# Kernel tuning notes

Hardware: AMD Instinct MI355X
Metric: run time of the kernel (lower is better)

The kernel has to match this reference:

```python
import jax, jax.numpy as jnp
import numpy as np

B, T, D = 4, 2048, 1024
H = 16
HD = D // H  # 64

def setup_inputs() -> dict:
    key = jax.random.key(0)
    ks = jax.random.split(key, 5)
    x = jax.random.normal(ks[0], (B, T, D), dtype=jnp.float32)
    # Linear params, torch default init scale ~ U(-1/sqrt(fan_in), 1/sqrt(fan_in))
    s = 1.0 / np.sqrt(D)
    W_qkv = jax.random.uniform(ks[1], (D, 3 * D), jnp.float32, -s, s)
    b_qkv = jax.random.uniform(ks[2], (3 * D,), jnp.float32, -s, s)
    W_proj = jax.random.uniform(ks[3], (D, D), jnp.float32, -s, s)
    b_proj = jax.random.uniform(ks[4], (D,), jnp.float32, -s, s)
    return {"x": x, "W_qkv": W_qkv, "b_qkv": b_qkv, "W_proj": W_proj, "b_proj": b_proj}

def reference(x, W_qkv, b_qkv, W_proj, b_proj):
    b, t, c = x.shape
    qkv = x @ W_qkv + b_qkv                       # [B,T,3D]
    q, k, v = jnp.split(qkv, 3, axis=-1)
    # [B,T,D] -> [B,H,T,HD]
    def heads(a):
        return a.reshape(b, t, H, HD).transpose(0, 2, 1, 3)
    q, k, v = heads(q), heads(k), heads(v)
    scale = 1.0 / jnp.sqrt(jnp.float32(HD))
    att = jnp.einsum('bhqd,bhkd->bhqk', q, k) * scale   # [B,H,T,T]
    causal = jnp.tril(jnp.ones((t, t), dtype=bool))
    att = jnp.where(causal, att, -jnp.inf)
    att = jax.nn.softmax(att, axis=-1)
    out = jnp.einsum('bhqk,bhkd->bhqd', att, v)          # [B,H,T,HD]
    out = out.transpose(0, 2, 1, 3).reshape(b, t, c)
    return out @ W_proj + b_proj
```

## Files before the change

kernel.cpp:

```cpp
#include <hip/hip_runtime.h>
#include <hip/hip_bf16.h>
#include <stdint.h>

using u16 = unsigned short;
using u32t = unsigned int;
typedef __bf16 bf16x8 __attribute__((ext_vector_type(8)));
typedef float f32x4 __attribute__((ext_vector_type(4)));
typedef float f32x16 __attribute__((ext_vector_type(16)));

#define SEQ_T 2048
#define DM 1024
#define NH 16
#define HD 64
#define NB 4

__device__ inline u16 f2bfu(float f) {
    __hip_bfloat16 h = __float2bfloat16(f);
    return __builtin_bit_cast(u16, h);
}

__device__ inline bf16x8 ld_frag(const u16* p) {
    return __builtin_bit_cast(bf16x8, *reinterpret_cast<const uint4*>(p));
}

__device__ inline void gload_lds16(const u16* g, u16* l) {
    __builtin_amdgcn_global_load_lds(
        (const __attribute__((address_space(1))) void*)g,
        (__attribute__((address_space(3))) void*)l, 16, 0, 0);
}

__device__ inline float fexp2(float x) { return __builtin_amdgcn_exp2f(x); }

__global__ __launch_bounds__(256) void prep_kernel(const float* __restrict__ x,
                                                   u16* __restrict__ xb,
                                                   const float* __restrict__ Wqkv,
                                                   u16* __restrict__ wtq,
                                                   const float* __restrict__ Wproj,
                                                   u16* __restrict__ wtp) {
    __shared__ __align__(16) float tile[64][72];
    const int bid = blockIdx.x;
    const int tid = threadIdx.x;
    if (bid < 4096) {
        size_t i = (size_t)bid * 256 + tid;
        const float4* xv = reinterpret_cast<const float4*>(x);
        float4 a = xv[2 * i];
        float4 b = xv[2 * i + 1];
        u16 r[8] = {f2bfu(a.x), f2bfu(a.y), f2bfu(a.z), f2bfu(a.w),
                    f2bfu(b.x), f2bfu(b.y), f2bfu(b.z), f2bfu(b.w)};
        *reinterpret_cast<uint4*>(xb + i * 8) = *reinterpret_cast<const uint4*>(r);
        return;
    }
    const float* W;
    u16* Wt;
    int N, t;
    if (bid < 4864) {
        W = Wqkv; Wt = wtq; N = 3072; t = bid - 4096;
    } else {
        W = Wproj; Wt = wtp; N = 1024; t = bid - 4864;
    }
    const int nbx = N >> 6;
    const int n0 = (t % nbx) * 64, k0 = (t / nbx) * 64;
    const int K = 1024;
#pragma unroll
    for (int p = 0; p < 4; ++p) {
        int idx = p * 256 + tid;
        int r = idx >> 4, c = (idx & 15) * 4;
        float4 v = *reinterpret_cast<const float4*>(&W[(size_t)(k0 + r) * N + n0 + c]);
        *reinterpret_cast<float4*>(&tile[r][c]) = v;
    }
    __syncthreads();
#pragma unroll
    for (int p = 0; p < 4; ++p) {
        int idx = p * 256 + tid;
        int nr = idx >> 4, kg = (idx & 15) * 4;
        u16 u[4];
#pragma unroll
        for (int j = 0; j < 4; ++j) u[j] = f2bfu(tile[kg + j][nr]);
        *reinterpret_cast<uint2*>(&Wt[(size_t)(n0 + nr) * K + k0 + kg]) =
            *reinterpret_cast<const uint2*>(u);
    }
}

template <int F32OUT, int SCALEQ>
__global__ __launch_bounds__(512, 2) void gemm_r3(const u16* __restrict__ A,
                                                  const u16* __restrict__ Bt,
                                                  const float* __restrict__ bias,
                                                  float* __restrict__ Cf,
                                                  u16* __restrict__ Cb,
                                                  int M, int N, int K) {
    __shared__ __align__(16) u16 smem[36864];
    const int tid = threadIdx.x;
    const int wid = tid >> 6, lane = tid & 63;
    const int llo = lane & 15, lhi = lane >> 4;
    const int wm = wid >> 1, wn = wid & 1;
    const int cpx = gridDim.x >> 3;
    const int swz = (blockIdx.x & 7) * cpx + (blockIdx.x >> 3);
    const int nb = N >> 7;
    const int m0 = (swz / nb) << 8, n0 = (swz % nb) << 7;
    const int T = K >> 5;

    f32x4 acc[4][4];
#pragma unroll
    for (int i = 0; i < 4; ++i)
#pragma unroll
        for (int j = 0; j < 4; ++j) acc[i][j] = (f32x4){0.f, 0.f, 0.f, 0.f};

    auto stage = [&](int t, int sb) {
        const int kb = t << 5;
#pragma unroll
        for (int j = 0; j < 2; ++j) {
            int c = j * 512 + tid;
            int row = c >> 2, kc = (c & 3) * 8;
            gload_lds16(A + (size_t)(m0 + row) * K + kb + kc, smem + sb + c * 8);
        }
        {
            int c = tid;
            int row = c >> 2, kc = (c & 3) * 8;
            gload_lds16(Bt + (size_t)(n0 + row) * K + kb + kc,
                        smem + sb + 8192 + c * 8);
        }
    };

    stage(0, 0);
    stage(1, 12288);

    for (int t = 0; t < T; ++t) {
        if (t == T - 1)
            asm volatile("s_waitcnt vmcnt(0)" ::: "memory");
        else
            asm volatile("s_waitcnt vmcnt(3)" ::: "memory");
        __builtin_amdgcn_sched_barrier(0);
        __builtin_amdgcn_s_barrier();
        __builtin_amdgcn_sched_barrier(0);
        const u16* Ab = smem + (t % 3) * 12288;
        const u16* Bb = Ab + 8192;
        bf16x8 af[4], bfr[4];
#pragma unroll
        for (int mf = 0; mf < 4; ++mf)
            af[mf] = ld_frag(Ab + (wm * 64 + mf * 16 + llo) * 32 + lhi * 8);
#pragma unroll
        for (int nf = 0; nf < 4; ++nf)
            bfr[nf] = ld_frag(Bb + (wn * 64 + nf * 16 + llo) * 32 + lhi * 8);
        if (t + 2 < T) stage(t + 2, ((t + 2) % 3) * 12288);
        __builtin_amdgcn_s_setprio(1);
#pragma unroll
        for (int mf = 0; mf < 4; ++mf)
#pragma unroll
            for (int nf = 0; nf < 4; ++nf)
                acc[mf][nf] = __builtin_amdgcn_mfma_f32_16x16x32_bf16(
                    af[mf], bfr[nf], acc[mf][nf], 0, 0, 0);
        __builtin_amdgcn_s_setprio(0);
    }

    const float SC2 = 0.18033688f;
    const int row_base = m0 + wm * 64;
    const int col_base = n0 + wn * 64;
#pragma unroll
    for (int nf = 0; nf < 4; ++nf) {
        int col = col_base + nf * 16 + llo;
        float bv = bias[col];
        const bool doScale = SCALEQ && (col < 1024);
#pragma unroll
        for (int mf = 0; mf < 4; ++mf) {
#pragma unroll
            for (int r = 0; r < 4; ++r) {
                int row = row_base + mf * 16 + lhi * 4 + r;
                float v = acc[mf][nf][r] + bv;
                if (doScale) v *= SC2;
                if (F32OUT)
                    Cf[(size_t)row * N + col] = v;
                else
                    Cb[(size_t)row * N + col] = f2bfu(v);
            }
        }
    }
}

template <int F32OUT, int SCALEQ>
__global__ __launch_bounds__(256, 3) void gemm_r4(const u16* __restrict__ A,
                                                  const u16* __restrict__ Bt,
                                                  const float* __restrict__ bias,
                                                  float* __restrict__ Cf,
                                                  u16* __restrict__ Cb,
                                                  int M, int N, int K) {
    __shared__ __align__(16) u16 smem[24576];
    const int tid = threadIdx.x;
    const int wid = tid >> 6, lane = tid & 63;
    const int llo = lane & 15, lhi = lane >> 4;
    const int wm = wid >> 1, wn = wid & 1;
    const int cpx = gridDim.x >> 3;
    const int swz = (blockIdx.x & 7) * cpx + (blockIdx.x >> 3);
    const int nb = N >> 7;
    const int m0 = (swz / nb) << 7, n0 = (swz % nb) << 7;
    const int T = K >> 5;

    f32x4 acc[4][4];
#pragma unroll
    for (int i = 0; i < 4; ++i)
#pragma unroll
        for (int j = 0; j < 4; ++j) acc[i][j] = (f32x4){0.f, 0.f, 0.f, 0.f};

    auto stage = [&](int t, int sb) {
        const int kb = t << 5;
#pragma unroll
        for (int j = 0; j < 2; ++j) {
            int c = j * 256 + tid;
            int row = c >> 2, kc = (c & 3) * 8;
            gload_lds16(A + (size_t)(m0 + row) * K + kb + kc, smem + sb + c * 8);
        }
#pragma unroll
        for (int j = 0; j < 2; ++j) {
            int c = j * 256 + tid;
            int row = c >> 2, kc = (c & 3) * 8;
            gload_lds16(Bt + (size_t)(n0 + row) * K + kb + kc,
                        smem + sb + 4096 + c * 8);
        }
    };

    stage(0, 0);
    stage(1, 8192);

    for (int t = 0; t < T; ++t) {
        if (t == T - 1)
            asm volatile("s_waitcnt vmcnt(0)" ::: "memory");
        else
            asm volatile("s_waitcnt vmcnt(4)" ::: "memory");
        __builtin_amdgcn_sched_barrier(0);
        __builtin_amdgcn_s_barrier();
        __builtin_amdgcn_sched_barrier(0);
        const u16* Ab = smem + (t % 3) * 8192;
        const u16* Bb = Ab + 4096;
        bf16x8 af[4], bfr[4];
#pragma unroll
        for (int mf = 0; mf < 4; ++mf)
            af[mf] = ld_frag(Ab + (wm * 64 + mf * 16 + llo) * 32 + lhi * 8);
#pragma unroll
        for (int nf = 0; nf < 4; ++nf)
            bfr[nf] = ld_frag(Bb + (wn * 64 + nf * 16 + llo) * 32 + lhi * 8);
        if (t + 2 < T) stage(t + 2, ((t + 2) % 3) * 8192);
        __builtin_amdgcn_s_setprio(1);
#pragma unroll
        for (int mf = 0; mf < 4; ++mf)
#pragma unroll
            for (int nf = 0; nf < 4; ++nf)
                acc[mf][nf] = __builtin_amdgcn_mfma_f32_16x16x32_bf16(
                    af[mf], bfr[nf], acc[mf][nf], 0, 0, 0);
        __builtin_amdgcn_s_setprio(0);
    }

    const float SC2 = 0.18033688f;
    const int row_base = m0 + wm * 64;
    const int col_base = n0 + wn * 64;
#pragma unroll
    for (int nf = 0; nf < 4; ++nf) {
        int col = col_base + nf * 16 + llo;
        float bv = bias[col];
        const bool doScale = SCALEQ && (col < 1024);
#pragma unroll
        for (int mf = 0; mf < 4; ++mf) {
#pragma unroll
            for (int r = 0; r < 4; ++r) {
                int row = row_base + mf * 16 + lhi * 4 + r;
                float v = acc[mf][nf][r] + bv;
                if (doScale) v *= SC2;
                if (F32OUT)
                    Cf[(size_t)row * N + col] = v;
                else
                    Cb[(size_t)row * N + col] = f2bfu(v);
            }
        }
    }
}

__global__ __launch_bounds__(512, 2) void attn_kernel(const u16* __restrict__ qkv,
                                                      u16* __restrict__ o) {
    __shared__ __align__(16) u16 smem[34048];
    const int bid = blockIdx.x;
    const int amap[8] = {7, 5, 3, 1, 6, 4, 2, 0};
    const int bh = bid & 63;
    const int qc = amap[bid >> 6];
    const int b = bh >> 4, h = bh & 15;
    const int tid = threadIdx.x;
    const int wid = tid >> 6, lane = tid & 63;
    const int l31 = lane & 31, lh = lane >> 5;
    const u16* base = qkv + (size_t)b * SEQ_T * (3 * DM);
    const int qrow0 = qc * 256 + wid * 32;
    const int q_abs = qrow0 + l31;
    const int nkv2 = 2 * qc + 2;

    bf16x8 qf[4];
    {
        const u16* qp = base + (size_t)q_abs * (3 * DM) + h * HD + lh * 8;
#pragma unroll
        for (int km = 0; km < 4; ++km) qf[km] = ld_frag(qp + km * 16);
    }

    f32x16 oac0, oac1;
#pragma unroll
    for (int r = 0; r < 16; ++r) { oac0[r] = 0.f; oac1[r] = 0.f; }
    float m_run = -1e30f, l_run = 0.f;

    uint4 va, vb;
    const int vpr = tid >> 3, vm = tid & 7;

    auto stageK = [&](int kb2, int bi2) {
#pragma unroll
        for (int p = 0; p < 2; ++p) {
            int kv = p * 64 + wid * 8 + (lane >> 3);
            int cl = lane & 7;
            const u16* src = base + (size_t)(kb2 * 128 + kv) * (3 * DM) + DM + h * HD +
                             ((cl ^ (kv & 7)) * 8);
            gload_lds16(src, smem + bi2 * 8320 + (p * 8 + wid) * 520);
        }
    };
    auto loadV = [&](int kb2) {
        const u16* vp =
            base + (size_t)(kb2 * 128 + 2 * vpr) * (3 * DM) + 2 * DM + h * HD + vm * 8;
        va = *reinterpret_cast<const uint4*>(vp);
        vb = *reinterpret_cast<const uint4*>(vp + 3 * DM);
    };
    auto writeV = [&](int bi2) {
        u16 ua[8], ub[8];
        *reinterpret_cast<uint4*>(ua) = va;
        *reinterpret_cast<uint4*>(ub) = vb;
        const int cbk = vpr >> 2, off = 2 * (vpr & 3);
        const int sw = (2 * vm) & 7;
        u16* vt = smem + 16640 + bi2 * 8704;
#pragma unroll
        for (int j = 0; j < 8; ++j) {
            int d = vm * 8 + j;
            u32t val = (u32t)ua[j] | ((u32t)ub[j] << 16);
            *reinterpret_cast<u32t*>(vt + d * 136 + ((cbk ^ sw) * 8) + off) = val;
        }
    };

    loadV(0);
    stageK(0, 0);
    writeV(0);
    asm volatile("s_waitcnt lgkmcnt(0)" ::: "memory");
    asm volatile("s_waitcnt vmcnt(1)" ::: "memory");
    __builtin_amdgcn_sched_barrier(0);
    __builtin_amdgcn_s_barrier();
    __builtin_amdgcn_sched_barrier(0);

    const int vsw = (2 * (l31 >> 3)) & 7;
    const int qmax = qrow0 + 31;
    const int krow0 = (l31 >> 3) * 520 + (l31 & 7) * 64;
    const int krow1 = (4 + (l31 >> 3)) * 520 + (l31 & 7) * 64;

    for (int kb2 = 0; kb2 < nkv2; ++kb2) {
        const int cur = kb2 & 1;
        const bool pre = (kb2 + 1 < nkv2);
        if (pre) { loadV(kb2 + 1); stageK(kb2 + 1, cur ^ 1); }

#pragma unroll
        for (int s = 0; s < 2; ++s) {
            if (s == 1) {
                if (pre) asm volatile("s_waitcnt vmcnt(4)" ::: "memory");
                else     asm volatile("s_waitcnt vmcnt(0)" ::: "memory");
                __builtin_amdgcn_sched_barrier(0);
            }
            const int kv0 = kb2 * 128 + s * 64;
            if (kv0 > qmax) continue;
            f32x16 s0, s1;
#pragma unroll
            for (int r = 0; r < 16; ++r) { s0[r] = 0.f; s1[r] = 0.f; }
            const u16* kbase = smem + cur * 8320 + s * 4160;
            __builtin_amdgcn_s_setprio(1);
#pragma unroll
            for (int km = 0; km < 4; ++km) {
                bf16x8 kf = ld_frag(kbase + krow0 + (((km * 2 + lh) ^ (l31 & 7)) * 8));
                s0 = __builtin_amdgcn_mfma_f32_32x32x16_bf16(kf, qf[km], s0, 0, 0, 0);
            }
#pragma unroll
            for (int km = 0; km < 4; ++km) {
                bf16x8 kf = ld_frag(kbase + krow1 + (((km * 2 + lh) ^ (l31 & 7)) * 8));
                s1 = __builtin_amdgcn_mfma_f32_32x32x16_bf16(kf, qf[km], s1, 0, 0, 0);
            }
            __builtin_amdgcn_s_setprio(0);

            if (kv0 + 63 > qrow0) {
#pragma unroll
                for (int r = 0; r < 16; ++r) {
                    int ka = kv0 + (r & 3) + 8 * (r >> 2) + 4 * lh;
                    if (ka > q_abs) s0[r] = -1e30f;
                    if (ka + 32 > q_abs) s1[r] = -1e30f;
                }
            }

            float t16[16];
#pragma unroll
            for (int r = 0; r < 16; ++r) t16[r] = fmaxf(s0[r], s1[r]);
#pragma unroll
            for (int r = 0; r < 8; ++r) t16[r] = fmaxf(t16[r], t16[r + 8]);
#pragma unroll
            for (int r = 0; r < 4; ++r) t16[r] = fmaxf(t16[r], t16[r + 4]);
            float pm = fmaxf(fmaxf(t16[0], t16[1]), fmaxf(t16[2], t16[3]));
            pm = fmaxf(pm, __shfl_xor(pm, 32));
            if (!__all(pm - m_run <= 8.f)) {
                const float mnew = fmaxf(m_run, pm);
                const float sc = fexp2(m_run - mnew);
                m_run = mnew;
                l_run *= sc;
#pragma unroll
                for (int r = 0; r < 16; ++r) { oac0[r] *= sc; oac1[r] *= sc; }
            }
            float a16[16];
#pragma unroll
            for (int r = 0; r < 16; ++r) { s0[r] = fexp2(s0[r] - m_run); }
#pragma unroll
            for (int r = 0; r < 16; ++r) { s1[r] = fexp2(s1[r] - m_run); }
#pragma unroll
            for (int r = 0; r < 16; ++r) a16[r] = s0[r] + s1[r];
#pragma unroll
            for (int r = 0; r < 8; ++r) a16[r] += a16[r + 8];
#pragma unroll
            for (int r = 0; r < 4; ++r) a16[r] += a16[r + 4];
            float sum = (a16[0] + a16[1]) + (a16[2] + a16[3]);
            sum += __shfl_xor(sum, 32);
            l_run += sum;

            u32t pk0[8], pk1[8];
#pragma unroll
            for (int w = 0; w < 8; ++w) {
                float a0 = s0[2 * w], b0 = s0[2 * w + 1];
                float a1 = s1[2 * w], b1 = s1[2 * w + 1];
                asm("v_cvt_pk_bf16_f32 %0, %1, %2" : "=v"(pk0[w]) : "v"(a0), "v"(b0));
                asm("v_cvt_pk_bf16_f32 %0, %1, %2" : "=v"(pk1[w]) : "v"(a1), "v"(b1));
            }
            asm("v_permlane32_swap_b32 %0, %1" : "+v"(pk0[0]), "+v"(pk0[2]));
            asm("v_permlane32_swap_b32 %0, %1" : "+v"(pk0[1]), "+v"(pk0[3]));
            asm("v_permlane32_swap_b32 %0, %1" : "+v"(pk0[4]), "+v"(pk0[6]));
            asm("v_permlane32_swap_b32 %0, %1" : "+v"(pk0[5]), "+v"(pk0[7]));
            asm("v_permlane32_swap_b32 %0, %1" : "+v"(pk1[0]), "+v"(pk1[2]));
            asm("v_permlane32_swap_b32 %0, %1" : "+v"(pk1[1]), "+v"(pk1[3]));
            asm("v_permlane32_swap_b32 %0, %1" : "+v"(pk1[4]), "+v"(pk1[6]));
            asm("v_permlane32_swap_b32 %0, %1" : "+v"(pk1[5]), "+v"(pk1[7]));
            bf16x8 pf[4];
            {
                uint4 t0 = {pk0[0], pk0[1], pk0[2], pk0[3]};
                uint4 t1 = {pk0[4], pk0[5], pk0[6], pk0[7]};
                uint4 t2 = {pk1[0], pk1[1], pk1[2], pk1[3]};
                uint4 t3 = {pk1[4], pk1[5], pk1[6], pk1[7]};
                pf[0] = __builtin_bit_cast(bf16x8, t0);
                pf[1] = __builtin_bit_cast(bf16x8, t1);
                pf[2] = __builtin_bit_cast(bf16x8, t2);
                pf[3] = __builtin_bit_cast(bf16x8, t3);
            }

            const u16* vbase = smem + 16640 + cur * 8704;
            __builtin_amdgcn_s_setprio(1);
#pragma unroll
            for (int km = 0; km < 4; ++km) {
                bf16x8 vf = ld_frag(vbase + l31 * 136 +
                                    ((s * 8 + ((km * 2 + lh) ^ vsw)) * 8));
                oac0 = __builtin_amdgcn_mfma_f32_32x32x16_bf16(vf, pf[km], oac0, 0, 0, 0);
            }
#pragma unroll
            for (int km = 0; km < 4; ++km) {
                bf16x8 vf = ld_frag(vbase + (32 + l31) * 136 +
                                    ((s * 8 + ((km * 2 + lh) ^ vsw)) * 8));
                oac1 = __builtin_amdgcn_mfma_f32_32x32x16_bf16(vf, pf[km], oac1, 0, 0, 0);
            }
            __builtin_amdgcn_s_setprio(0);
        }

        if (pre) {
            writeV(cur ^ 1);
            asm volatile("s_waitcnt lgkmcnt(0)" ::: "memory");
            asm volatile("s_waitcnt vmcnt(1)" ::: "memory");
        } else {
            asm volatile("s_waitcnt lgkmcnt(0)" ::: "memory");
        }
        __builtin_amdgcn_sched_barrier(0);
        __builtin_amdgcn_s_barrier();
        __builtin_amdgcn_sched_barrier(0);
    }

    const float inv = 1.f / l_run;
    u16* osh = smem + wid * 2240;
#pragma unroll
    for (int r = 0; r < 16; ++r) {
        int dl = (r & 3) + 8 * (r >> 2) + 4 * lh;
        osh[l31 * 70 + dl] = f2bfu(oac0[r] * inv);
        osh[l31 * 70 + 32 + dl] = f2bfu(oac1[r] * inv);
    }
    __syncthreads();
    {
        const u16* rs = osh + l31 * 70 + lh * 32;
        u16* op = o + (size_t)(b * SEQ_T + qrow0 + l31) * DM + h * HD + lh * 32;
        u32t w[16];
#pragma unroll
        for (int i = 0; i < 16; ++i) w[i] = *reinterpret_cast<const u32t*>(rs + i * 2);
#pragma unroll
        for (int i = 0; i < 4; ++i) {
            uint4 t = {w[4 * i], w[4 * i + 1], w[4 * i + 2], w[4 * i + 3]};
            *reinterpret_cast<uint4*>(op + 8 * i) = t;
        }
    }
}

extern "C" void kernel_launch(void* const* d_in, const int* in_sizes, int n_in,
                              void* d_out, int out_size, void* d_ws, size_t ws_size,
                              hipStream_t stream) {
    const float* x = (const float*)d_in[0];
    const float* Wqkv = (const float*)d_in[1];
    const float* bqkv = (const float*)d_in[2];
    const float* Wproj = (const float*)d_in[3];
    const float* bproj = (const float*)d_in[4];
    float* out = (float*)d_out;
    char* ws = (char*)d_ws;

    u16* xb   = (u16*)(ws);
    u16* wtq  = (u16*)(ws + 16777216);
    u16* wtp  = (u16*)(ws + 23068672);
    u16* qkvb = (u16*)(ws + 25165824);
    u16* ob   = (u16*)(ws + 75497472);

    prep_kernel<<<5120, 256, 0, stream>>>(x, xb, Wqkv, wtq, Wproj, wtp);

    gemm_r3<0, 1><<<768, 512, 0, stream>>>(
        xb, wtq, bqkv, nullptr, qkvb, 8192, 3072, 1024);

    attn_kernel<<<512, 512, 0, stream>>>(qkvb, ob);

    gemm_r4<1, 0><<<512, 256, 0, stream>>>(
        ob, wtp, bproj, out, nullptr, 8192, 1024, 1024);
}
```

Before: 160.5 us.

## Split KV range of long causal query chunks and merge with combine kernel

Query chunks 4–7, which have the longest causal KV ranges, are each split into two blocks covering halves of the KV range. Each half writes an unnormalized bf16 partial output plus its running max and sum. A new combine kernel rescales and merges the two halves. The goal is to even out per-block work across the 768-block grid and cut the tail from the heaviest causal chunks. The cost is an extra launch and extra partial-output traffic through workspace that reuses the x and W_qkv staging buffers.

```diff
diff --git a/kernel.cpp b/kernel.cpp
--- a/kernel.cpp
+++ b/kernel.cpp
@@ -273,20 +273,33 @@
 }
 
 __global__ __launch_bounds__(512, 2) void attn_kernel(const u16* __restrict__ qkv,
-                                                      u16* __restrict__ o) {
+                                                      u16* __restrict__ o,
+                                                      u16* __restrict__ pO,
+                                                      float* __restrict__ pm,
+                                                      float* __restrict__ pl) {
     __shared__ __align__(16) u16 smem[34048];
+    const int jmap[12] = {3, 10, 11, 8, 9, 2, 6, 7, 4, 5, 1, 0};
     const int bid = blockIdx.x;
-    const int amap[8] = {7, 5, 3, 1, 6, 4, 2, 0};
+    const int j = jmap[bid >> 6];
     const int bh = bid & 63;
-    const int qc = amap[bid >> 6];
     const int b = bh >> 4, h = bh & 15;
+    int qc, kb_lo, kb_hi, sidx = -1;
+    if (j < 4) {
+        qc = j; kb_lo = 0; kb_hi = 2 * j + 2;
+    } else {
+        qc = 4 + ((j - 4) >> 1);
+        const int part = (j - 4) & 1;
+        const int hh = qc + 1;
+        kb_lo = part ? hh : 0;
+        kb_hi = part ? 2 * qc + 2 : hh;
+        sidx = (bh * 4 + (qc - 4)) * 2 + part;
+    }
     const int tid = threadIdx.x;
     const int wid = tid >> 6, lane = tid & 63;
     const int l31 = lane & 31, lh = lane >> 5;
     const u16* base = qkv + (size_t)b * SEQ_T * (3 * DM);
     const int qrow0 = qc * 256 + wid * 32;
     const int q_abs = qrow0 + l31;
-    const int nkv2 = 2 * qc + 2;
 
     bf16x8 qf[4];
     {
@@ -327,15 +340,15 @@
         const int sw = (2 * vm) & 7;
         u16* vt = smem + 16640 + bi2 * 8704;
 #pragma unroll
-        for (int j = 0; j < 8; ++j) {
-            int d = vm * 8 + j;
-            u32t val = (u32t)ua[j] | ((u32t)ub[j] << 16);
+        for (int jj = 0; jj < 8; ++jj) {
+            int d = vm * 8 + jj;
+            u32t val = (u32t)ua[jj] | ((u32t)ub[jj] << 16);
             *reinterpret_cast<u32t*>(vt + d * 136 + ((cbk ^ sw) * 8) + off) = val;
         }
     };
 
-    loadV(0);
-    stageK(0, 0);
+    loadV(kb_lo);
+    stageK(kb_lo, 0);
     writeV(0);
     asm volatile("s_waitcnt lgkmcnt(0)" ::: "memory");
     asm volatile("s_waitcnt vmcnt(1)" ::: "memory");
@@ -348,9 +361,9 @@
     const int krow0 = (l31 >> 3) * 520 + (l31 & 7) * 64;
     const int krow1 = (4 + (l31 >> 3)) * 520 + (l31 & 7) * 64;
 
-    for (int kb2 = 0; kb2 < nkv2; ++kb2) {
-        const int cur = kb2 & 1;
-        const bool pre = (kb2 + 1 < nkv2);
+    for (int kb2 = kb_lo; kb2 < kb_hi; ++kb2) {
+        const int cur = (kb2 - kb_lo) & 1;
+        const bool pre = (kb2 + 1 < kb_hi);
         if (pre) { loadV(kb2 + 1); stageK(kb2 + 1, cur ^ 1); }
 
 #pragma unroll
@@ -395,10 +408,10 @@
             for (int r = 0; r < 8; ++r) t16[r] = fmaxf(t16[r], t16[r + 8]);
 #pragma unroll
             for (int r = 0; r < 4; ++r) t16[r] = fmaxf(t16[r], t16[r + 4]);
-            float pm = fmaxf(fmaxf(t16[0], t16[1]), fmaxf(t16[2], t16[3]));
-            pm = fmaxf(pm, __shfl_xor(pm, 32));
-            if (!__all(pm - m_run <= 8.f)) {
-                const float mnew = fmaxf(m_run, pm);
+            float pmx = fmaxf(fmaxf(t16[0], t16[1]), fmaxf(t16[2], t16[3]));
+            pmx = fmaxf(pmx, __shfl_xor(pmx, 32));
+            if (!__all(pmx - m_run <= 8.f)) {
+                const float mnew = fmaxf(m_run, pmx);
                 const float sc = fexp2(m_run - mnew);
                 m_run = mnew;
                 l_run *= sc;
@@ -477,16 +490,16 @@
         __builtin_amdgcn_sched_barrier(0);
     }
 
-    const float inv = 1.f / l_run;
     u16* osh = smem + wid * 2240;
-#pragma unroll
-    for (int r = 0; r < 16; ++r) {
-        int dl = (r & 3) + 8 * (r >> 2) + 4 * lh;
-        osh[l31 * 70 + dl] = f2bfu(oac0[r] * inv);
-        osh[l31 * 70 + 32 + dl] = f2bfu(oac1[r] * inv);
-    }
-    __syncthreads();
-    {
+    if (sidx < 0) {
+        const float inv = 1.f / l_run;
+#pragma unroll
+        for (int r = 0; r < 16; ++r) {
+            int dl = (r & 3) + 8 * (r >> 2) + 4 * lh;
+            osh[l31 * 70 + dl] = f2bfu(oac0[r] * inv);
+            osh[l31 * 70 + 32 + dl] = f2bfu(oac1[r] * inv);
+        }
+        __syncthreads();
         const u16* rs = osh + l31 * 70 + lh * 32;
         u16* op = o + (size_t)(b * SEQ_T + qrow0 + l31) * DM + h * HD + lh * 32;
         u32t w[16];
@@ -497,7 +510,69 @@
             uint4 t = {w[4 * i], w[4 * i + 1], w[4 * i + 2], w[4 * i + 3]};
             *reinterpret_cast<uint4*>(op + 8 * i) = t;
         }
-    }
+    } else {
+#pragma unroll
+        for (int r = 0; r < 16; ++r) {
+            int dl = (r & 3) + 8 * (r >> 2) + 4 * lh;
+            osh[l31 * 70 + dl] = f2bfu(oac0[r]);
+            osh[l31 * 70 + 32 + dl] = f2bfu(oac1[r]);
+        }
+        if (lh == 0) {
+            pm[sidx * 256 + wid * 32 + l31] = m_run;
+            pl[sidx * 256 + wid * 32 + l31] = l_run;
+        }
+        __syncthreads();
+        const u16* rs = osh + l31 * 70 + lh * 32;
+        u16* op = pO + ((size_t)sidx * 256 + wid * 32 + l31) * 64 + lh * 32;
+        u32t w[16];
+#pragma unroll
+        for (int i = 0; i < 16; ++i) w[i] = *reinterpret_cast<const u32t*>(rs + i * 2);
+#pragma unroll
+        for (int i = 0; i < 4; ++i) {
+            uint4 t = {w[4 * i], w[4 * i + 1], w[4 * i + 2], w[4 * i + 3]};
+            *reinterpret_cast<uint4*>(op + 8 * i) = t;
+        }
+    }
+}
+
+__global__ __launch_bounds__(256) void combine_kernel(const u16* __restrict__ pO,
+                                                      const float* __restrict__ pm,
+                                                      const float* __restrict__ pl,
+                                                      u16* __restrict__ ob) {
+    const int bid = blockIdx.x;
+    const int bh = bid >> 2, qci = bid & 3;
+    const int qc = qci + 4;
+    const int b = bh >> 4, h = bh & 15;
+    const int q = threadIdx.x;
+    const int ia = ((bh * 4 + qci) * 2 + 0) * 256 + q;
+    const int ib = ((bh * 4 + qci) * 2 + 1) * 256 + q;
+    float mA = pm[ia], mB = pm[ib];
+    float lA = pl[ia], lB = pl[ib];
+    float m = fmaxf(mA, mB);
+    float cA = fexp2(mA - m), cB = fexp2(mB - m);
+    float rinv = 1.f / (lA * cA + lB * cB);
+    cA *= rinv;
+    cB *= rinv;
+    const u16* pa = pO + (size_t)ia * 64;
+    const u16* pb = pO + (size_t)ib * 64;
+    u16* op = ob + (size_t)(b * SEQ_T + qc * 256 + q) * DM + h * HD;
+    u16 outb[64];
+#pragma unroll
+    for (int c = 0; c < 8; ++c) {
+        u16 ua[8], ub[8];
+        *reinterpret_cast<uint4*>(ua) = *reinterpret_cast<const uint4*>(pa + c * 8);
+        *reinterpret_cast<uint4*>(ub) = *reinterpret_cast<const uint4*>(pb + c * 8);
+#pragma unroll
+        for (int e = 0; e < 8; ++e) {
+            float fa = __builtin_bit_cast(float, (u32t)ua[e] << 16);
+            float fb = __builtin_bit_cast(float, (u32t)ub[e] << 16);
+            outb[c * 8 + e] = f2bfu(fa * cA + fb * cB);
+        }
+    }
+#pragma unroll
+    for (int c = 0; c < 8; ++c)
+        *reinterpret_cast<uint4*>(op + c * 8) =
+            *reinterpret_cast<const uint4*>(outb + c * 8);
 }
 
 extern "C" void kernel_launch(void* const* d_in, const int* in_sizes, int n_in,
@@ -516,13 +591,17 @@
     u16* wtp  = (u16*)(ws + 23068672);
     u16* qkvb = (u16*)(ws + 25165824);
     u16* ob   = (u16*)(ws + 75497472);
+    u16*   pO = (u16*)(ws);
+    float* pm = (float*)(ws + 16777216);
+    float* pl = (float*)(ws + 16777216 + 524288);
 
     prep_kernel<<<5120, 256, 0, stream>>>(x, xb, Wqkv, wtq, Wproj, wtp);
 
     gemm_r3<0, 1><<<768, 512, 0, stream>>>(
         xb, wtq, bqkv, nullptr, qkvb, 8192, 3072, 1024);
 
-    attn_kernel<<<512, 512, 0, stream>>>(qkvb, ob);
+    attn_kernel<<<768, 512, 0, stream>>>(qkvb, ob, pO, pm, pl);
+    combine_kernel<<<256, 256, 0, stream>>>(pO, pm, pl, ob);
 
     gemm_r4<1, 0><<<512, 256, 0, stream>>>(
         ob, wtp, bproj, out, nullptr, 8192, 1024, 1024);
```

Result: slower. 176.7 us (+10.1%).
